# Kernel tuning notes

Hardware: AMD Instinct MI355X
Metric: run time of the kernel (lower is better)

The kernel has to match this reference:

```python
import jax, jax.numpy as jnp
import numpy as np

B, S, D = 4, 2048, 1024
H, DH = 16, 64  # d_model = H*DH = 1024
NEG = 1e10


def setup_inputs() -> dict:
    key = jax.random.key(0)
    ks = jax.random.split(key, 5)
    scale = 1.0 / np.sqrt(D)
    x = jax.random.normal(ks[0], (B, S, D), dtype=jnp.float32)
    mask = jax.random.randint(ks[1], (B, S), 0, 2).astype(jnp.float32)
    Wq = jax.random.normal(ks[2], (D, H * DH), dtype=jnp.float32) * scale
    Wk = jax.random.normal(ks[3], (D, H * DH), dtype=jnp.float32) * scale
    Wv = jax.random.normal(ks[4], (D, H * DH), dtype=jnp.float32) * scale
    z = jnp.zeros((H * DH,), dtype=jnp.float32)
    return {"x": x, "mask": mask, "Wq": Wq, "bq": z, "Wk": Wk, "bk": z,
            "Wv": Wv, "bv": z}


def reference(x, mask, Wq, bq, Wk, bk, Wv, bv):
    # projections -> [B, H, S, DH]
    def proj(W, b):
        y = x @ W + b
        return y.reshape(B, S, H, DH).transpose(0, 2, 1, 3)

    q, k, v = proj(Wq, bq), proj(Wk, bk), proj(Wv, bv)
    scores = jnp.einsum("bhsd,bhtd->bhst", q, k) / np.sqrt(DH)
    m = mask[:, None, None, :]                      # [B,1,1,S]
    scores = scores - (1.0 - m) * NEG               # additive mask
    probs = jax.nn.softmax(scores, axis=-1)         # stable (max-subtract)
    probs = probs * m                               # multiplicative mask
    out = jnp.einsum("bhst,bhtd->bhsd", probs, v)   # [B,H,S,DH]
    return out.transpose(0, 2, 1, 3).reshape(B, S, H * DH)
```

## Files before the change

### kernel.cpp

```cpp
#include <hip/hip_runtime.h>

typedef float f32x4 __attribute__((ext_vector_type(4)));
typedef float f32x16 __attribute__((ext_vector_type(16)));
typedef _Float16 f16;
typedef _Float16 f16x2 __attribute__((ext_vector_type(2)));
typedef _Float16 f16x8 __attribute__((ext_vector_type(8)));
typedef unsigned int u32x2 __attribute__((ext_vector_type(2)));
typedef unsigned short u16;
typedef unsigned short u16x4 __attribute__((ext_vector_type(4)));
typedef unsigned int u32;

#define S_LEN 2048
#define NHEAD 16
#define DHEAD 64
#define DMODEL 1024
#define NBATCH 4

__device__ __forceinline__ void gload16(const u16* g, const uint4* l) {
  __builtin_amdgcn_global_load_lds((const __attribute__((address_space(1))) void*)g,
                                   (__attribute__((address_space(3))) void*)l, 16, 0, 0);
}


__device__ __forceinline__ float dot2acc(u32 a, u32 b, float c) {
#if __has_builtin(__builtin_amdgcn_fdot2)
  return __builtin_amdgcn_fdot2(__builtin_bit_cast(f16x2, a), __builtin_bit_cast(f16x2, b), c, false);
#else
  f16x2 pa = __builtin_bit_cast(f16x2, a), pb = __builtin_bit_cast(f16x2, b);
  return c + (float)pa[0] * (float)pb[0] + (float)pa[1] * (float)pb[1];
#endif
}

__global__ void cvt_x(const float* __restrict__ x, u16* __restrict__ o, int n4) {
  int i = blockIdx.x * blockDim.x + threadIdx.x;
  int st = gridDim.x * blockDim.x;
  for (; i < n4; i += st) {
    float4 v = reinterpret_cast<const float4*>(x)[i];
    uint2 r;
    r.x = __builtin_bit_cast(u32, __builtin_amdgcn_cvt_pkrtz(v.x, v.y));
    r.y = __builtin_bit_cast(u32, __builtin_amdgcn_cvt_pkrtz(v.z, v.w));
    reinterpret_cast<uint2*>(o)[i] = r;
  }
}

__global__ void trans_w(const float* __restrict__ W, u16* __restrict__ wt) {
  __shared__ float t[32][33];
  int bx = blockIdx.x * 32, by = blockIdx.y * 32;
  int tx = threadIdx.x & 31, ty = threadIdx.x >> 5;
#pragma unroll
  for (int i = 0; i < 32; i += 8)
    t[ty + i][tx] = W[(size_t)(by + ty + i) * DMODEL + bx + tx];
  __syncthreads();
#pragma unroll
  for (int i = 0; i < 32; i += 8)
    wt[(size_t)(bx + ty + i) * DMODEL + by + tx] = __builtin_bit_cast(u16, (f16)t[tx][ty + i]);
}

__global__ __launch_bounds__(256) void qkv_gemm(
    const u16* __restrict__ A, const u16* __restrict__ Wt,
    const float* __restrict__ bq, const float* __restrict__ bk, const float* __restrict__ bv,
    const float* __restrict__ mask,
    u16* __restrict__ Qo, u16* __restrict__ Ko, u16* __restrict__ Vo)
{
  __shared__ uint4 As4[3][512];
  __shared__ uint4 Bs4[3][512];
  const int tid = threadIdx.x;
  const int lane = tid & 63;
  const int wid = tid >> 6;
  const int l31 = lane & 31, hi = lane >> 5;
  const int m0 = blockIdx.x * 128;
  const int n0 = blockIdx.y * 128;
  const int wr = (wid >> 1) * 64, wc = (wid & 1) * 64;

  f32x16 acc[2][2] = {};

  const int c0 = wid * 64 + lane, c1 = c0 + 256;
  const int r0 = c0 >> 2, r1 = c1 >> 2;
  const int p4 = lane & 3;
  const int sl0 = p4 ^ ((r0 >> 1) & 3);
  const int sl1 = p4 ^ ((r1 >> 1) & 3);
  const u16* ag0 = A  + (size_t)(m0 + r0) * 1024 + sl0 * 8;
  const u16* ag1 = A  + (size_t)(m0 + r1) * 1024 + sl1 * 8;
  const u16* bg0 = Wt + (size_t)(n0 + r0) * 1024 + sl0 * 8;
  const u16* bg1 = Wt + (size_t)(n0 + r1) * 1024 + sl1 * 8;

  auto stage = [&](int buf, int kt) {
    gload16(ag0 + kt, &As4[buf][wid * 64]);
    gload16(ag1 + kt, &As4[buf][wid * 64 + 256]);
    gload16(bg0 + kt, &Bs4[buf][wid * 64]);
    gload16(bg1 + kt, &Bs4[buf][wid * 64 + 256]);
  };

  int aoff[2][2], boff[2][2];
#pragma unroll
  for (int mi = 0; mi < 2; mi++) {
    int r = wr + mi * 32 + l31;
#pragma unroll
    for (int ks = 0; ks < 2; ks++)
      aoff[mi][ks] = r * 32 + (((ks * 2 + hi) ^ ((r >> 1) & 3)) * 8);
  }
#pragma unroll
  for (int ni = 0; ni < 2; ni++) {
    int r = wc + ni * 32 + l31;
#pragma unroll
    for (int ks = 0; ks < 2; ks++)
      boff[ni][ks] = r * 32 + (((ks * 2 + hi) ^ ((r >> 1) & 3)) * 8);
  }

  stage(0, 0);
  stage(1, 32);
  __syncthreads();

  const int NT = 1024 / 32;
  for (int it = 0; it < NT; ++it) {
    if (it + 1 < NT) asm volatile("s_waitcnt vmcnt(4)" ::: "memory");
    else             asm volatile("s_waitcnt vmcnt(0)" ::: "memory");
    __builtin_amdgcn_s_barrier();
    __builtin_amdgcn_sched_barrier(0);
    const int cur = it % 3;
    if (it + 2 < NT) stage((it + 2) % 3, (it + 2) * 32);

    const u16* As = (const u16*)&As4[cur][0];
    const u16* Bs = (const u16*)&Bs4[cur][0];
    f16x8 af[2][2], bf[2][2];
#pragma unroll
    for (int mi = 0; mi < 2; mi++)
#pragma unroll
      for (int ks = 0; ks < 2; ks++)
        af[mi][ks] = *(const f16x8*)&As[aoff[mi][ks]];
#pragma unroll
    for (int ni = 0; ni < 2; ni++)
#pragma unroll
      for (int ks = 0; ks < 2; ks++)
        bf[ni][ks] = *(const f16x8*)&Bs[boff[ni][ks]];

#pragma unroll
    for (int ks = 0; ks < 2; ks++)
#pragma unroll
      for (int mi = 0; mi < 2; mi++)
#pragma unroll
        for (int ni = 0; ni < 2; ni++)
          acc[mi][ni] = __builtin_amdgcn_mfma_f32_32x32x16_f16(af[mi][ks], bf[ni][ks], acc[mi][ni], 0, 0, 0);
  }

  const int sel = n0 >> 10;
  const float* bias = (sel == 0) ? bq : (sel == 1) ? bk : bv;
  const int nbase = (n0 & 1023) + wc;
  const float QSCALE = 0.18033688011112042f;
#pragma unroll
  for (int mi = 0; mi < 2; mi++)
#pragma unroll
    for (int ni = 0; ni < 2; ni++) {
      const int ncol = nbase + ni * 32 + l31;
      const float bi = bias[ncol];
      const int h = ncol >> 6, dh = ncol & 63;
#pragma unroll
      for (int r4 = 0; r4 < 4; r4++) {
        const int rowb = m0 + wr + mi * 32 + 8 * r4 + 4 * hi;
        const int bb = rowb >> 11, s0 = rowb & 2047;
        const size_t bh = (size_t)(bb * NHEAD + h);
        if (sel == 0) {
#pragma unroll
          for (int j = 0; j < 4; j++)
            Qo[(bh * S_LEN + s0 + j) * DHEAD + dh] =
                __builtin_bit_cast(u16, (f16)((acc[mi][ni][r4 * 4 + j] + bi) * QSCALE));
        } else if (sel == 1) {
#pragma unroll
          for (int j = 0; j < 4; j++)
            Ko[(bh * S_LEN + s0 + j) * DHEAD + dh] =
                __builtin_bit_cast(u16, (f16)(acc[mi][ni][r4 * 4 + j] + bi));
        } else {
          const float4 mk = *(const float4*)&mask[bb * S_LEN + s0];
          u16x4 pk;
#pragma unroll
          for (int j = 0; j < 4; j++) {
            float v = acc[mi][ni][r4 * 4 + j] + bi;
            float mj = (j == 0) ? mk.x : (j == 1) ? mk.y : (j == 2) ? mk.z : mk.w;
            if (mj <= 0.f) v = 0.f;
            pk[j] = __builtin_bit_cast(u16, (f16)v);
          }
          *(u16x4*)&Vo[(bh * DHEAD + dh) * S_LEN + s0] = pk;
        }
      }
    }
}

__global__ __launch_bounds__(256, 2) void attn(
    const u16* __restrict__ Q, const u16* __restrict__ K, const u16* __restrict__ Vt,
    const float* __restrict__ mask, float* __restrict__ out)
{
  __shared__ uint4 Ks4[3][512];
  __shared__ uint4 Vs4[3][512];
  __shared__ __align__(16) u16 MsAll[S_LEN];
  const int tid = threadIdx.x;
  const int lane = tid & 63, wid = tid >> 6;
  const int l31 = lane & 31, hi = lane >> 5;
  const int sid = blockIdx.x;
  const int qt = (sid >> 3) & 7;
  const int bh = (sid & 7) + 8 * (sid >> 6);
  const int b = bh >> 4, h = bh & 15;
  const size_t base = (size_t)bh * S_LEN * DHEAD;
  const u16* Qp = Q + base;
  const u16* Kp = K + base;
  const u16* Vp = Vt + base;
  const float* mp = mask + b * S_LEN;
  const int q0 = qt * 256 + wid * 64;

  f16x8 aqA[4], aqB[4];
#pragma unroll
  for (int kc = 0; kc < 4; kc++) {
    aqA[kc] = *(const f16x8*)&Qp[(size_t)(q0 + l31) * DHEAD + kc * 16 + hi * 8];
    aqB[kc] = *(const f16x8*)&Qp[(size_t)(q0 + 32 + l31) * DHEAD + kc * 16 + hi * 8];
  }

  f32x16 accO0A = {}, accO1A = {};
  f32x16 accO0B = {}, accO1B = {};
  float lAp[4] = {0.f, 0.f, 0.f, 0.f};
  float lBp[4] = {0.f, 0.f, 0.f, 0.f};

  const int cA_ = wid * 128 + lane, cB_ = cA_ + 64;
  const int rk0 = cA_ >> 3, rk1 = cB_ >> 3;
  const int p8 = lane & 7;
  const int cc0 = (p8 - ((rk0 + (rk0 >> 3)) & 7)) & 7;
  const int cc1 = (p8 - ((rk1 + (rk1 >> 3)) & 7)) & 7;
  const u16* kg0 = Kp + (size_t)rk0 * DHEAD + cc0 * 8;
  const u16* kg1 = Kp + (size_t)rk1 * DHEAD + cc1 * 8;
  const u16* vg0 = Vp + (size_t)rk0 * S_LEN + cc0 * 8;
  const u16* vg1 = Vp + (size_t)rk1 * S_LEN + cc1 * 8;

  auto stage = [&](int buf) {
    gload16(kg0, &Ks4[buf][wid * 128]); gload16(kg1, &Ks4[buf][wid * 128 + 64]);
    gload16(vg0, &Vs4[buf][wid * 128]); gload16(vg1, &Vs4[buf][wid * 128 + 64]);
    kg0 += 64 * DHEAD; kg1 += 64 * DHEAD; vg0 += 64; vg1 += 64;
  };

  const int swA = (l31 + (l31 >> 3)) & 7;
  const int swB = (swA + 4) & 7;
  int idxA[4], idxB[4];
#pragma unroll
  for (int kc = 0; kc < 4; kc++) {
    idxA[kc] = l31 * 8 + ((kc * 2 + hi + swA) & 7);
    idxB[kc] = (32 + l31) * 8 + ((kc * 2 + hi + swB) & 7);
  }

  {
    float4 ml0 = *(const float4*)&mp[tid * 8];
    float4 ml1 = *(const float4*)&mp[tid * 8 + 4];
    uint4 w;
    w.x = __builtin_bit_cast(u32, __builtin_amdgcn_cvt_pkrtz(ml0.x, ml0.y));
    w.y = __builtin_bit_cast(u32, __builtin_amdgcn_cvt_pkrtz(ml0.z, ml0.w));
    w.z = __builtin_bit_cast(u32, __builtin_amdgcn_cvt_pkrtz(ml1.x, ml1.y));
    w.w = __builtin_bit_cast(u32, __builtin_amdgcn_cvt_pkrtz(ml1.z, ml1.w));
    *(uint4*)&MsAll[tid * 8] = w;
  }
  stage(0);
  stage(1);
  __syncthreads();

  f32x16 pA0 = {}, pA1 = {}, pB0 = {}, pB1 = {};

  auto qkt = [&](const uint4* ks, f32x16& A0, f32x16& A1, f32x16& B0, f32x16& B1) {
#pragma unroll
    for (int kc = 0; kc < 4; kc++) {
      f16x8 k0 = *(const f16x8*)&ks[idxA[kc]];
      f16x8 k1 = *(const f16x8*)&ks[idxB[kc]];
      A0 = __builtin_amdgcn_mfma_f32_32x32x16_f16(k0, aqA[kc], A0, 0, 0, 0);
      A1 = __builtin_amdgcn_mfma_f32_32x32x16_f16(k1, aqA[kc], A1, 0, 0, 0);
      B0 = __builtin_amdgcn_mfma_f32_32x32x16_f16(k0, aqB[kc], B0, 0, 0, 0);
      B1 = __builtin_amdgcn_mfma_f32_32x32x16_f16(k1, aqB[kc], B1, 0, 0, 0);
    }
  };

  auto phaseB = [&](const uint4* vs, int it) {
#pragma unroll
    for (int g = 0; g < 4; g++) {
      const f32x16& srcA = (g < 2) ? pA0 : pA1;
      const f32x16& srcB = (g < 2) ? pB0 : pB1;
      const int o = (g & 1) * 8;
      u32 wa[4], wb[4];
#pragma unroll
      for (int s = 0; s < 4; s++) {
        wa[s] = __builtin_bit_cast(u32, __builtin_amdgcn_cvt_pkrtz(
                    __builtin_amdgcn_exp2f(srcA[o + 2 * s]),
                    __builtin_amdgcn_exp2f(srcA[o + 2 * s + 1])));
        wb[s] = __builtin_bit_cast(u32, __builtin_amdgcn_cvt_pkrtz(
                    __builtin_amdgcn_exp2f(srcB[o + 2 * s]),
                    __builtin_amdgcn_exp2f(srcB[o + 2 * s + 1])));
      }
      u32x2 rA0 = __builtin_amdgcn_permlane32_swap(wa[0], wa[2], false, false);
      u32x2 rA1 = __builtin_amdgcn_permlane32_swap(wa[1], wa[3], false, false);
      u32x2 rB0 = __builtin_amdgcn_permlane32_swap(wb[0], wb[2], false, false);
      u32x2 rB1 = __builtin_amdgcn_permlane32_swap(wb[1], wb[3], false, false);
      uint4 f4A; f4A.x = rA0[0]; f4A.y = rA1[0]; f4A.z = rA0[1]; f4A.w = rA1[1];
      uint4 f4B; f4B.x = rB0[0]; f4B.y = rB1[0]; f4B.z = rB0[1]; f4B.w = rB1[1];
      f16x8 fA = __builtin_bit_cast(f16x8, f4A);
      f16x8 fB = __builtin_bit_cast(f16x8, f4B);
      f16x8 bv0 = *(const f16x8*)&vs[idxA[g]];
      f16x8 bv1 = *(const f16x8*)&vs[idxB[g]];
      const uint4 bmw = *(const uint4*)&MsAll[it * 64 + g * 16 + hi * 8];
      accO0A = __builtin_amdgcn_mfma_f32_32x32x16_f16(fA, bv0, accO0A, 0, 0, 0);
      accO1A = __builtin_amdgcn_mfma_f32_32x32x16_f16(fA, bv1, accO1A, 0, 0, 0);
      accO0B = __builtin_amdgcn_mfma_f32_32x32x16_f16(fB, bv0, accO0B, 0, 0, 0);
      accO1B = __builtin_amdgcn_mfma_f32_32x32x16_f16(fB, bv1, accO1B, 0, 0, 0);
      lAp[0] = dot2acc(f4A.x, bmw.x, lAp[0]);
      lAp[1] = dot2acc(f4A.y, bmw.y, lAp[1]);
      lAp[2] = dot2acc(f4A.z, bmw.z, lAp[2]);
      lAp[3] = dot2acc(f4A.w, bmw.w, lAp[3]);
      lBp[0] = dot2acc(f4B.x, bmw.x, lBp[0]);
      lBp[1] = dot2acc(f4B.y, bmw.y, lBp[1]);
      lBp[2] = dot2acc(f4B.z, bmw.z, lBp[2]);
      lBp[3] = dot2acc(f4B.w, bmw.w, lBp[3]);
    }
  };

  qkt(&Ks4[0][0], pA0, pA1, pB0, pB1);

  const int NT = S_LEN / 64;
  for (int it = 0; it < NT - 1; ++it) {
    asm volatile("s_waitcnt vmcnt(0)" ::: "memory");
    __builtin_amdgcn_s_barrier();
    __builtin_amdgcn_sched_barrier(0);
    const int cur = it % 3, nxt = (it + 1) % 3;
    if (it + 2 < NT) stage((it + 2) % 3);
    f32x16 nA0 = {}, nA1 = {}, nB0 = {}, nB1 = {};
    qkt(&Ks4[nxt][0], nA0, nA1, nB0, nB1);
    phaseB(&Vs4[cur][0], it);
    pA0 = nA0; pA1 = nA1; pB0 = nB0; pB1 = nB1;
  }
  phaseB(&Vs4[(NT - 1) % 3][0], NT - 1);

  float lA = (lAp[0] + lAp[1]) + (lAp[2] + lAp[3]);
  float lB = (lBp[0] + lBp[1]) + (lBp[2] + lBp[3]);
  float lAf = lA + __shfl_xor(lA, 32, 64);
  float lBf = lB + __shfl_xor(lB, 32, 64);
  float invA = (lAf > 0.f) ? 1.f / lAf : 0.f;
  float invB = (lBf > 0.f) ? 1.f / lBf : 0.f;
#pragma unroll
  for (int r = 0; r < 16; r++) {
    int qr = (r & 3) + 8 * (r >> 2) + 4 * hi;
    float iA = __builtin_bit_cast(float,
        (u32)__builtin_amdgcn_ds_bpermute(qr << 2, (int)__builtin_bit_cast(u32, invA)));
    float iB = __builtin_bit_cast(float,
        (u32)__builtin_amdgcn_ds_bpermute(qr << 2, (int)__builtin_bit_cast(u32, invB)));
    float* opA = out + ((size_t)(b * S_LEN + q0 + qr) * DMODEL) + h * DHEAD;
    float* opB = out + ((size_t)(b * S_LEN + q0 + 32 + qr) * DMODEL) + h * DHEAD;
    opA[l31] = accO0A[r] * iA;
    opA[32 + l31] = accO1A[r] * iA;
    opB[l31] = accO0B[r] * iB;
    opB[32 + l31] = accO1B[r] * iB;
  }
}

extern "C" void kernel_launch(void* const* d_in, const int* in_sizes, int n_in,
                              void* d_out, int out_size, void* d_ws, size_t ws_size,
                              hipStream_t stream) {
  const float* x    = (const float*)d_in[0];
  const float* mask = (const float*)d_in[1];
  const float* Wq   = (const float*)d_in[2];
  const float* bq   = (const float*)d_in[3];
  const float* Wk   = (const float*)d_in[4];
  const float* bk   = (const float*)d_in[5];
  const float* Wv   = (const float*)d_in[6];
  const float* bv   = (const float*)d_in[7];
  float* out = (float*)d_out;

  u16* xb = (u16*)d_ws;
  u16* wt = xb + (size_t)8192 * 1024;
  u16* Qb = wt + (size_t)3072 * 1024;
  u16* Kb = Qb + (size_t)8388608;
  u16* Vb = Kb + (size_t)8388608;

  cvt_x<<<2048, 256, 0, stream>>>(x, xb, (8192 * 1024) / 4);
  trans_w<<<dim3(32, 32), 256, 0, stream>>>(Wq, wt);
  trans_w<<<dim3(32, 32), 256, 0, stream>>>(Wk, wt + (size_t)1024 * 1024);
  trans_w<<<dim3(32, 32), 256, 0, stream>>>(Wv, wt + (size_t)2 * 1024 * 1024);
  qkv_gemm<<<dim3(64, 24), 256, 0, stream>>>(xb, wt, bq, bk, bv, mask, Qb, Kb, Vb);
  attn<<<512, 256, 0, stream>>>(Qb, Kb, Vb, mask, out);
}
```

Measured before the change: 168.1 us.

## Load K tiles directly into registers and drop LDS staging for K

K tiles are no longer staged through shared memory. Each lane now loads its MFMA operand fragments straight from global memory into registers, one tile ahead. The software pipeline that overlapped the next tile's QK^T with the current PV is replaced by a plain loop that computes QK^T and then PV for the same tile. This removes the LDS traffic and footprint for K, but adds uncoalesced-ish global loads, more register pressure, and less overlap between the two MFMA phases.

```diff
diff --git a/kernel.cpp b/kernel.cpp
--- a/kernel.cpp
+++ b/kernel.cpp
@@ -189,7 +189,6 @@
     const u16* __restrict__ Q, const u16* __restrict__ K, const u16* __restrict__ Vt,
     const float* __restrict__ mask, float* __restrict__ out)
 {
-  __shared__ uint4 Ks4[3][512];
   __shared__ uint4 Vs4[3][512];
   __shared__ __align__(16) u16 MsAll[S_LEN];
   const int tid = threadIdx.x;
@@ -223,15 +222,12 @@
   const int p8 = lane & 7;
   const int cc0 = (p8 - ((rk0 + (rk0 >> 3)) & 7)) & 7;
   const int cc1 = (p8 - ((rk1 + (rk1 >> 3)) & 7)) & 7;
-  const u16* kg0 = Kp + (size_t)rk0 * DHEAD + cc0 * 8;
-  const u16* kg1 = Kp + (size_t)rk1 * DHEAD + cc1 * 8;
   const u16* vg0 = Vp + (size_t)rk0 * S_LEN + cc0 * 8;
   const u16* vg1 = Vp + (size_t)rk1 * S_LEN + cc1 * 8;
 
   auto stage = [&](int buf) {
-    gload16(kg0, &Ks4[buf][wid * 128]); gload16(kg1, &Ks4[buf][wid * 128 + 64]);
     gload16(vg0, &Vs4[buf][wid * 128]); gload16(vg1, &Vs4[buf][wid * 128 + 64]);
-    kg0 += 64 * DHEAD; kg1 += 64 * DHEAD; vg0 += 64; vg1 += 64;
+    vg0 += 64; vg1 += 64;
   };
 
   const int swA = (l31 + (l31 >> 3)) & 7;
@@ -242,6 +238,8 @@
     idxA[kc] = l31 * 8 + ((kc * 2 + hi + swA) & 7);
     idxB[kc] = (32 + l31) * 8 + ((kc * 2 + hi + swB) & 7);
   }
+
+  const u16* kq = Kp + l31 * DHEAD + hi * 8;
 
   {
     float4 ml0 = *(const float4*)&mp[tid * 8];
@@ -255,27 +253,46 @@
   }
   stage(0);
   stage(1);
+  f16x8 kr[4][2];
+#pragma unroll
+  for (int kc = 0; kc < 4; kc++) {
+    kr[kc][0] = *(const f16x8*)(kq + kc * 16);
+    kr[kc][1] = *(const f16x8*)(kq + 2048 + kc * 16);
+  }
   __syncthreads();
 
-  f32x16 pA0 = {}, pA1 = {}, pB0 = {}, pB1 = {};
-
-  auto qkt = [&](const uint4* ks, f32x16& A0, f32x16& A1, f32x16& B0, f32x16& B1) {
+  const int NT = S_LEN / 64;
+  for (int it = 0; it < NT; ++it) {
+    asm volatile("s_waitcnt vmcnt(0)" ::: "memory");
+    __builtin_amdgcn_s_barrier();
+    __builtin_amdgcn_sched_barrier(0);
+    const int cur = it % 3;
+    const uint4* vs = &Vs4[cur][0];
+    if (it + 2 < NT) stage((it + 2) % 3);
+
+    f16x8 krn[4][2];
+    if (it + 1 < NT) {
+      const u16* kqn = kq + (it + 1) * 4096;
+#pragma unroll
+      for (int kc = 0; kc < 4; kc++) {
+        krn[kc][0] = *(const f16x8*)(kqn + kc * 16);
+        krn[kc][1] = *(const f16x8*)(kqn + 2048 + kc * 16);
+      }
+    }
+
+    f32x16 sA0 = {}, sA1 = {}, sB0 = {}, sB1 = {};
 #pragma unroll
     for (int kc = 0; kc < 4; kc++) {
-      f16x8 k0 = *(const f16x8*)&ks[idxA[kc]];
-      f16x8 k1 = *(const f16x8*)&ks[idxB[kc]];
-      A0 = __builtin_amdgcn_mfma_f32_32x32x16_f16(k0, aqA[kc], A0, 0, 0, 0);
-      A1 = __builtin_amdgcn_mfma_f32_32x32x16_f16(k1, aqA[kc], A1, 0, 0, 0);
-      B0 = __builtin_amdgcn_mfma_f32_32x32x16_f16(k0, aqB[kc], B0, 0, 0, 0);
-      B1 = __builtin_amdgcn_mfma_f32_32x32x16_f16(k1, aqB[kc], B1, 0, 0, 0);
+      sA0 = __builtin_amdgcn_mfma_f32_32x32x16_f16(kr[kc][0], aqA[kc], sA0, 0, 0, 0);
+      sA1 = __builtin_amdgcn_mfma_f32_32x32x16_f16(kr[kc][1], aqA[kc], sA1, 0, 0, 0);
+      sB0 = __builtin_amdgcn_mfma_f32_32x32x16_f16(kr[kc][0], aqB[kc], sB0, 0, 0, 0);
+      sB1 = __builtin_amdgcn_mfma_f32_32x32x16_f16(kr[kc][1], aqB[kc], sB1, 0, 0, 0);
     }
-  };
-
-  auto phaseB = [&](const uint4* vs, int it) {
+
 #pragma unroll
     for (int g = 0; g < 4; g++) {
-      const f32x16& srcA = (g < 2) ? pA0 : pA1;
-      const f32x16& srcB = (g < 2) ? pB0 : pB1;
+      const f32x16& srcA = (g < 2) ? sA0 : sA1;
+      const f32x16& srcB = (g < 2) ? sB0 : sB1;
       const int o = (g & 1) * 8;
       u32 wa[4], wb[4];
 #pragma unroll
@@ -311,23 +328,10 @@
       lBp[2] = dot2acc(f4B.z, bmw.z, lBp[2]);
       lBp[3] = dot2acc(f4B.w, bmw.w, lBp[3]);
     }
-  };
-
-  qkt(&Ks4[0][0], pA0, pA1, pB0, pB1);
-
-  const int NT = S_LEN / 64;
-  for (int it = 0; it < NT - 1; ++it) {
-    asm volatile("s_waitcnt vmcnt(0)" ::: "memory");
-    __builtin_amdgcn_s_barrier();
-    __builtin_amdgcn_sched_barrier(0);
-    const int cur = it % 3, nxt = (it + 1) % 3;
-    if (it + 2 < NT) stage((it + 2) % 3);
-    f32x16 nA0 = {}, nA1 = {}, nB0 = {}, nB1 = {};
-    qkt(&Ks4[nxt][0], nA0, nA1, nB0, nB1);
-    phaseB(&Vs4[cur][0], it);
-    pA0 = nA0; pA1 = nA1; pB0 = nB0; pB1 = nB1;
-  }
-  phaseB(&Vs4[(NT - 1) % 3][0], NT - 1);
+
+#pragma unroll
+    for (int kc = 0; kc < 4; kc++) { kr[kc][0] = krn[kc][0]; kr[kc][1] = krn[kc][1]; }
+  }
 
   float lA = (lAp[0] + lAp[1]) + (lAp[2] + lAp[3]);
   float lB = (lBp[0] + lBp[1]) + (lBp[2] + lBp[3]);
```

New measurement: 212.9 us. 26.7% more time.
